# Performance work log

Measured on AMD Instinct MI355X. Metric: run time of the kernel, lower is better.

Reference implementation:

```python
import jax, jax.numpy as jnp
import numpy as np

B, C, H, W = 8, 128, 64, 64

def conv2d(x, w, b, pad):
    # x: [B,C,H,W], w: [O,I,kh,kw] -> NCHW conv with symmetric padding
    y = jax.lax.conv_general_dilated(
        x, w, window_strides=(1, 1), padding=[(pad, pad), (pad, pad)],
        dimension_numbers=("NCHW", "OIHW", "NCHW"))
    return y + b[None, :, None, None]

def setup_inputs() -> dict:
    key = jax.random.key(0)
    ks = jax.random.split(key, 5)
    s3 = 1.0 / np.sqrt(C * 9)  # kaiming-uniform-ish scale for 3x3 conv
    s1 = 1.0 / np.sqrt(C)
    return {
        "x": jax.random.normal(ks[0], (B, C, H, W), jnp.float32),
        "Wq": jax.random.normal(ks[1], (C, C, 3, 3), jnp.float32) * s3,
        "bq": jnp.zeros((C,), jnp.float32),
        "Wk": jax.random.normal(ks[2], (C, C, 3, 3), jnp.float32) * s3,
        "bk": jnp.zeros((C,), jnp.float32),
        "Wv": jax.random.normal(ks[3], (C, C, 3, 3), jnp.float32) * s3,
        "bv": jnp.zeros((C,), jnp.float32),
        "Wo": jax.random.normal(ks[4], (C, C, 1, 1), jnp.float32) * s1,
        "bo": jnp.zeros((C,), jnp.float32),
    }

def reference(x, Wq, bq, Wk, bk, Wv, bv, Wo, bo):
    b, c, h, w = x.shape
    n = h * w
    scale = c ** (-0.5)
    # NOTE: original module defines self.norm but never applies it in forward.
    q = conv2d(x, Wq, bq, 1).reshape(b, c, n)
    k = conv2d(x, Wk, bk, 1).reshape(b, c, n)
    v = conv2d(x, Wv, bv, 1).reshape(b, c, n)
    attn = jax.nn.softmax(jnp.einsum("bci,bcj->bij", q, k) * scale, axis=2)  # [b,n,n]
    out = jnp.einsum("bij,bcj->bci", attn, v).reshape(b, c, h, w)
    out = conv2d(out, Wo, bo, 0)
    return x + out
```

## Files before the change

### kernel.cpp

```cpp
#include <hip/hip_runtime.h>

typedef __attribute__((ext_vector_type(8))) short bf16x8;
typedef __attribute__((ext_vector_type(4))) float f32x4;
typedef __attribute__((ext_vector_type(16))) float f32x16;

static __device__ __forceinline__ unsigned short f2bf(float f) {
    union { float f; unsigned int u; } v; v.f = f;
    unsigned int r = v.u + 0x7FFFu + ((v.u >> 16) & 1u);
    return (unsigned short)(r >> 16);
}

static __device__ __forceinline__ unsigned cvtpk_bf16(float lo, float hi) {
    unsigned r;
    asm("v_cvt_pk_bf16_f32 %0, %1, %2" : "=v"(r) : "v"(lo), "v"(hi));
    return r;
}

#define NRW (27 * 16384)

__global__ __launch_bounds__(256) void repack_k(const float* __restrict__ Wq, const float* __restrict__ Wk,
                                                const float* __restrict__ Wv, const float* __restrict__ Wo,
                                                unsigned short* __restrict__ RW, unsigned short* __restrict__ WoB) {
    int t = blockIdx.x * 256 + threadIdx.x;
    if (t < NRW) {
        int s = t & 7, o = (t >> 3) & 127, g = (t >> 10) & 3, cc = (t >> 12) & 3, tap = t >> 14;
        int conv = tap / 9, kk = tap % 9, kh = kk / 3, kw = kk % 3;
        int c = cc * 32 + g * 8 + s;
        const float* W = (conv == 0) ? Wq : ((conv == 1) ? Wk : Wv);
        RW[t] = f2bf(W[((o * 128 + c) * 3 + kh) * 3 + kw]);
    } else {
        int u = t - NRW;
        if (u < 16384) WoB[u] = f2bf(Wo[u]);
    }
}

__global__ __launch_bounds__(256) void qkv_conv_k(const float* __restrict__ x, const unsigned short* __restrict__ RW,
                                                  const float* __restrict__ bq, const float* __restrict__ bk,
                                                  const float* __restrict__ bv,
                                                  unsigned short* __restrict__ q_ws, unsigned short* __restrict__ k_ws,
                                                  unsigned short* __restrict__ v_ws) {
    __shared__ unsigned short xs[3 * 66 * 128];
    const int tid = threadIdx.x;
    const int b = blockIdx.x >> 6, h = blockIdx.x & 63;
    for (int i = tid; i < 3 * 66 * 128; i += 256) xs[i] = 0;
    __syncthreads();
    for (int ch = tid; ch < 3 * 128 * 16; ch += 256) {
        int r3 = ch >> 11, rem = ch & 2047, c = rem >> 4, w4 = rem & 15;
        int hh = h - 1 + r3;
        if (hh >= 0 && hh < 64) {
            float4 v = *(const float4*)(x + ((b * 128 + c) * 64 + hh) * 64 + w4 * 4);
            float vv[4] = {v.x, v.y, v.z, v.w};
#pragma unroll
            for (int j = 0; j < 4; ++j) {
                int wr = w4 * 4 + j + 1;
                unsigned int byte = (unsigned int)(((r3 * 66 + wr) * 128 + c) * 2) ^ ((wr & 7) << 4);
                *(unsigned short*)((char*)xs + byte) = f2bf(vv[j]);
            }
        }
    }
    __syncthreads();
    const int lane = tid & 63, wave = tid >> 6;
    const int l15 = lane & 15, g = lane >> 4;
    f32x4 acc[4][6];
#pragma unroll
    for (int i = 0; i < 4; ++i)
#pragma unroll
        for (int j = 0; j < 6; ++j) acc[i][j] = (f32x4){0.f, 0.f, 0.f, 0.f};
#pragma unroll 1
    for (int kk = 0; kk < 9; ++kk) {
        const int kw = kk % 3;
#pragma unroll 2
        for (int cc = 0; cc < 4; ++cc) {
            bf16x8 a[4];
#pragma unroll
            for (int mf = 0; mf < 4; ++mf) {
                int wr = mf * 16 + l15 + kw;
                unsigned int byte = (unsigned int)((((kk / 3) * 66 + wr) * 128 + cc * 32 + g * 8) * 2) ^ ((wr & 7) << 4);
                a[mf] = *(const bf16x8*)((const char*)xs + byte);
            }
#pragma unroll
            for (int n6 = 0; n6 < 6; ++n6) {
                int nt = wave * 6 + n6;
                int conv = nt >> 3;
                int o = (nt * 16 + l15) & 127;
                bf16x8 bfr = *(const bf16x8*)(RW + ((((conv * 9 + kk) * 4 + cc) * 4 + g) * 128 + o) * 8);
#pragma unroll
                for (int mf = 0; mf < 4; ++mf)
                    acc[mf][n6] = __builtin_amdgcn_mfma_f32_16x16x32_bf16(a[mf], bfr, acc[mf][n6], 0, 0, 0);
            }
        }
    }
    const float SCALE2 = 0.08838834764831845f * 1.4426950408889634f;
#pragma unroll
    for (int n6 = 0; n6 < 6; ++n6) {
        int nt = wave * 6 + n6;
        int conv = nt >> 3;
        int o = (nt * 16 + l15) & 127;
        float bias = (conv == 0) ? bq[o] : ((conv == 1) ? bk[o] : bv[o]);
#pragma unroll
        for (int mf = 0; mf < 4; ++mf) {
#pragma unroll
            for (int r = 0; r < 4; ++r) {
                int pos = h * 64 + mf * 16 + g * 4 + r;
                float val = acc[mf][n6][r] + bias;
                if (conv == 0)      q_ws[(b * 4096 + pos) * 128 + o] = f2bf(val * SCALE2);
                else if (conv == 1) k_ws[(b * 4096 + pos) * 128 + o] = f2bf(val);
                else                v_ws[(b * 128 + o) * 4096 + pos] = f2bf(val);
            }
        }
    }
}

#define AS1C(p) ((const __attribute__((address_space(1))) void*)(p))
#define AS3(p)  ((__attribute__((address_space(3))) void*)(p))

__global__ __launch_bounds__(256, 2) void attn_k(
    const unsigned short* __restrict__ q_ws, const unsigned short* __restrict__ k_ws,
    const unsigned short* __restrict__ v_ws, const unsigned short* __restrict__ WoB,
    const float* __restrict__ bo, const float* __restrict__ x, float* __restrict__ out) {
    __shared__ __align__(16) char smem[66560];

    const int tid = threadIdx.x;
    const int lane = tid & 63, wave = tid >> 6;
    const int wj = wave & 1, wi = wave >> 1;
    const int l31 = lane & 31, h = lane >> 5;
    const int b = blockIdx.x & 7;
    const int qt = blockIdx.x >> 3;
    const int ibase = qt * 64;

    const char* kB = (const char*)(k_ws + (size_t)b * 4096 * 128);
    const char* vB = (const char*)(v_ws + (size_t)b * 128 * 4096);

    auto stage = [&](int buf, int kt) {
        char* Kn = smem + buf * 32768;
        char* Vn = Kn + 16384;
#pragma unroll
        for (int q = 0; q < 4; ++q) {
            int slot = (wave * 4 + q) * 64 + lane;
            int krow = slot >> 4, ks = slot & 15;
            int kcs = ks ^ (krow & 15);
            __builtin_amdgcn_global_load_lds(AS1C(kB + (size_t)(kt * 64 + krow) * 256 + kcs * 16),
                                             AS3(Kn + slot * 16), 16, 0, 0);
            int sr = slot >> 4, s8p = slot & 15;
            int s8 = s8p ^ (sr & 15);
            int crow = sr * 2 + (s8 >> 3), jch = s8 & 7;
            __builtin_amdgcn_global_load_lds(AS1C(vB + (size_t)crow * 8192 + kt * 128 + jch * 16),
                                             AS3(Vn + slot * 16), 16, 0, 0);
        }
    };

    stage(0, 0);

    bf16x8 qf[8];
    {
        const unsigned short* qrow = q_ws + ((size_t)b * 4096 + ibase + wi * 32 + l31) * 128;
#pragma unroll
        for (int cc = 0; cc < 8; ++cc) qf[cc] = *(const bf16x8*)(qrow + cc * 16 + h * 8);
    }

    f32x16 zero16;
#pragma unroll
    for (int r = 0; r < 16; ++r) zero16[r] = 0.f;
    f32x16 oac[4];
#pragma unroll
    for (int cf = 0; cf < 4; ++cf)
#pragma unroll
        for (int r = 0; r < 16; ++r) oac[cf][r] = 0.f;
    float m = -1e30f, ssum = 0.f;

    __syncthreads();

#pragma unroll 1
    for (int kt = 0; kt < 64; ++kt) {
        const int cur = kt & 1;
        const char* Kc = smem + cur * 32768;
        const char* Vc = Kc + 16384;
        if (kt < 63) stage(cur ^ 1, kt + 1);

        const int jrow = wj * 32 + l31;
        f32x16 st;
        __builtin_amdgcn_s_setprio(1);
        {
            unsigned byte = (unsigned)(jrow * 256 + ((h ^ (jrow & 15)) << 4));
            bf16x8 kf = *(const bf16x8*)(Kc + byte);
            st = __builtin_amdgcn_mfma_f32_32x32x16_bf16(kf, qf[0], zero16, 0, 0, 0);
        }
#pragma unroll
        for (int cc = 1; cc < 8; ++cc) {
            unsigned byte = (unsigned)(jrow * 256 + (((cc * 2 + h) ^ (jrow & 15)) << 4));
            bf16x8 kf = *(const bf16x8*)(Kc + byte);
            st = __builtin_amdgcn_mfma_f32_32x32x16_bf16(kf, qf[cc], st, 0, 0, 0);
        }
        __builtin_amdgcn_s_setprio(0);

        float x0 = fmaxf(fmaxf(st[0], st[1]), st[2]);
        float x1 = fmaxf(fmaxf(st[3], st[4]), st[5]);
        float x2 = fmaxf(fmaxf(st[6], st[7]), st[8]);
        float x3 = fmaxf(fmaxf(st[9], st[10]), st[11]);
        float x4 = fmaxf(fmaxf(st[12], st[13]), st[14]);
        float y0 = fmaxf(fmaxf(x0, x1), x2);
        float y1 = fmaxf(fmaxf(x3, x4), st[15]);
        float tmax = fmaxf(y0, y1);
        tmax = fmaxf(tmax, __shfl_xor(tmax, 32));
        if (!__all(tmax <= m + 8.f)) {
            float mnew = fmaxf(m, tmax);
            float corr = exp2f(m - mnew);
            ssum *= corr;
#pragma unroll
            for (int cf = 0; cf < 4; ++cf)
#pragma unroll
                for (int r = 0; r < 16; ++r) oac[cf][r] *= corr;
            m = mnew;
        }

        float ps = 0.f;
#pragma unroll
        for (int js = 0; js < 2; ++js) {
            float pA0 = exp2f(st[8 * js + 0] - m);
            float pA1 = exp2f(st[8 * js + 1] - m);
            float pA2 = exp2f(st[8 * js + 2] - m);
            float pA3 = exp2f(st[8 * js + 3] - m);
            float pB0 = exp2f(st[8 * js + 4] - m);
            float pB1 = exp2f(st[8 * js + 5] - m);
            float pB2 = exp2f(st[8 * js + 6] - m);
            float pB3 = exp2f(st[8 * js + 7] - m);
            ps += ((pA0 + pA1) + (pA2 + pA3)) + ((pB0 + pB1) + (pB2 + pB3));
            unsigned a0 = cvtpk_bf16(pA0, pA1), a1 = cvtpk_bf16(pA2, pA3);
            unsigned b0 = cvtpk_bf16(pB0, pB1), b1 = cvtpk_bf16(pB2, pB3);
            auto r0 = __builtin_amdgcn_permlane32_swap(a0, b0, false, false);
            auto r1 = __builtin_amdgcn_permlane32_swap(a1, b1, false, false);
            union { unsigned w[4]; bf16x8 v; } pu;
            pu.w[0] = r0[0];
            pu.w[1] = r1[0];
            pu.w[2] = r0[1];
            pu.w[3] = r1[1];
            const int jch = wj * 4 + js * 2 + h;
            __builtin_amdgcn_s_setprio(1);
#pragma unroll
            for (int cf = 0; cf < 4; ++cf) {
                int crow = cf * 32 + l31;
                int sr = crow >> 1;
                int s8 = ((crow & 1) << 3) | jch;
                unsigned vbyte = (unsigned)(sr * 256 + ((s8 ^ (sr & 15)) << 4));
                bf16x8 va = *(const bf16x8*)(Vc + vbyte);
                oac[cf] = __builtin_amdgcn_mfma_f32_32x32x16_bf16(va, pu.v, oac[cf], 0, 0, 0);
            }
            __builtin_amdgcn_s_setprio(0);
        }
        ps += __shfl_xor(ps, 32);
        ssum += ps;
        __syncthreads();
    }

    float* sRed = (float*)(smem + 65536);
    const int it = wi * 32 + l31;
    if (h == 0) {
        sRed[(wj * 64 + it) * 2] = m;
        sRed[(wj * 64 + it) * 2 + 1] = ssum;
    }
    __syncthreads();
    float m1 = sRed[((wj ^ 1) * 64 + it) * 2];
    float s1 = sRed[((wj ^ 1) * 64 + it) * 2 + 1];
    float M = fmaxf(m, m1);
    float aS = exp2f(m - M);
    float inv = 1.0f / (aS * ssum + exp2f(m1 - M) * s1);

    char* sBig = smem + 32768;
    if (wj == 1) {
#pragma unroll
        for (int cf = 0; cf < 4; ++cf)
#pragma unroll
            for (int g = 0; g < 4; ++g) {
                int c = cf * 32 + g * 8 + 4 * h;
                f32x4 v4;
#pragma unroll
                for (int k = 0; k < 4; ++k) v4[k] = aS * oac[cf][4 * g + k];
                unsigned byte = (unsigned)(it * 512 + c * 4) ^ ((it & 7) << 4);
                *(f32x4*)(sBig + byte) = v4;
            }
    }
    __syncthreads();
    unsigned short* sOut = (unsigned short*)smem;
    if (wj == 0) {
#pragma unroll
        for (int cf = 0; cf < 4; ++cf)
#pragma unroll
            for (int g = 0; g < 4; ++g) {
                int c = cf * 32 + g * 8 + 4 * h;
                unsigned rbyte = (unsigned)(it * 512 + c * 4) ^ ((it & 7) << 4);
                f32x4 rd = *(const f32x4*)((const char*)sBig + rbyte);
                float u0 = (aS * oac[cf][4 * g + 0] + rd[0]) * inv;
                float u1 = (aS * oac[cf][4 * g + 1] + rd[1]) * inv;
                float u2 = (aS * oac[cf][4 * g + 2] + rd[2]) * inv;
                float u3 = (aS * oac[cf][4 * g + 3] + rd[3]) * inv;
                uint2 pk;
                pk.x = cvtpk_bf16(u0, u1);
                pk.y = cvtpk_bf16(u2, u3);
                unsigned wbyte = (unsigned)(it * 256 + c * 2) ^ ((it & 15) << 4);
                *(uint2*)((char*)sOut + wbyte) = pk;
            }
    }
    __syncthreads();

#pragma unroll
    for (int t = 0; t < 2; ++t) {
        int tt = wave * 2 + t;
        int of = tt >> 1, ifl = tt & 1;
        int ir = ifl * 32 + l31;
        f32x16 acc;
#pragma unroll
        for (int r = 0; r < 16; ++r) acc[r] = 0.f;
#pragma unroll
        for (int cc = 0; cc < 8; ++cc) {
            unsigned bbyte = (unsigned)(ir * 256 + cc * 32 + h * 16) ^ ((ir & 15) << 4);
            bf16x8 bfr = *(const bf16x8*)((const char*)sOut + bbyte);
            bf16x8 wa = *(const bf16x8*)(WoB + (of * 32 + l31) * 128 + cc * 16 + h * 8);
            acc = __builtin_amdgcn_mfma_f32_32x32x16_bf16(wa, bfr, acc, 0, 0, 0);
        }
        int iglob = ibase + ir;
#pragma unroll
        for (int r = 0; r < 16; ++r) {
            int o = of * 32 + (r & 3) + 8 * (r >> 2) + 4 * h;
            size_t gidx = ((size_t)b * 128 + o) * 4096 + iglob;
            out[gidx] = acc[r] + bo[o] + x[gidx];
        }
    }
}

extern "C" void kernel_launch(void* const* d_in, const int* in_sizes, int n_in,
                              void* d_out, int out_size, void* d_ws, size_t ws_size,
                              hipStream_t stream) {
    const float* x  = (const float*)d_in[0];
    const float* Wq = (const float*)d_in[1];
    const float* bq = (const float*)d_in[2];
    const float* Wk = (const float*)d_in[3];
    const float* bk = (const float*)d_in[4];
    const float* Wv = (const float*)d_in[5];
    const float* bv = (const float*)d_in[6];
    const float* Wo = (const float*)d_in[7];
    const float* bo = (const float*)d_in[8];
    char* ws = (char*)d_ws;
    unsigned short* q_ws = (unsigned short*)(ws);
    unsigned short* k_ws = (unsigned short*)(ws + 8388608);
    unsigned short* v_ws = (unsigned short*)(ws + 16777216);
    unsigned short* RW   = (unsigned short*)(ws + 25165824);
    unsigned short* WoB  = (unsigned short*)(ws + 26050560);
    float* out = (float*)d_out;

    hipLaunchKernelGGL(repack_k, dim3(1792), dim3(256), 0, stream, Wq, Wk, Wv, Wo, RW, WoB);
    hipLaunchKernelGGL(qkv_conv_k, dim3(512), dim3(256), 0, stream, x, RW, bq, bk, bv, q_ws, k_ws, v_ws);
    hipLaunchKernelGGL(attn_k, dim3(512), dim3(256), 0, stream, q_ws, k_ws, v_ws, WoB, bo, x, out);
}
```

Measured before the change: 165.3 us.

## Software-pipeline QK^T one tile ahead and split K/V staging buffers

Restructures the attention loop so the QK^T MFMAs for tile kt+1 are issued before the softmax and PV work of tile kt. This gives the matrix units independent work to overlap with the exp and max VALU work. K is now prefetched two tiles ahead and V one tile ahead in separate double buffers, and the global addresses are precomputed once outside the loop. The s_setprio hints are removed. The change holds an extra 16-register score accumulator live, which raises register pressure and may limit occupancy at two blocks per CU.

```diff
diff --git a/kernel.cpp b/kernel.cpp
--- a/kernel.cpp
+++ b/kernel.cpp
@@ -131,25 +131,33 @@
     const char* kB = (const char*)(k_ws + (size_t)b * 4096 * 128);
     const char* vB = (const char*)(v_ws + (size_t)b * 128 * 4096);
 
-    auto stage = [&](int buf, int kt) {
-        char* Kn = smem + buf * 32768;
-        char* Vn = Kn + 16384;
-#pragma unroll
-        for (int q = 0; q < 4; ++q) {
-            int slot = (wave * 4 + q) * 64 + lane;
-            int krow = slot >> 4, ks = slot & 15;
-            int kcs = ks ^ (krow & 15);
-            __builtin_amdgcn_global_load_lds(AS1C(kB + (size_t)(kt * 64 + krow) * 256 + kcs * 16),
-                                             AS3(Kn + slot * 16), 16, 0, 0);
-            int sr = slot >> 4, s8p = slot & 15;
-            int s8 = s8p ^ (sr & 15);
-            int crow = sr * 2 + (s8 >> 3), jch = s8 & 7;
-            __builtin_amdgcn_global_load_lds(AS1C(vB + (size_t)crow * 8192 + kt * 128 + jch * 16),
-                                             AS3(Vn + slot * 16), 16, 0, 0);
-        }
+    const char* kgp[4]; const char* vgp[4]; int dst[4];
+#pragma unroll
+    for (int q = 0; q < 4; ++q) {
+        int slot = (wave * 4 + q) * 64 + lane;
+        int krow = slot >> 4, ks = slot & 15;
+        int kcs = ks ^ (krow & 15);
+        kgp[q] = kB + (size_t)krow * 256 + kcs * 16;
+        int sr = slot >> 4, s8p = slot & 15;
+        int s8 = s8p ^ (sr & 15);
+        int crow = sr * 2 + (s8 >> 3), jch = s8 & 7;
+        vgp[q] = vB + (size_t)crow * 8192 + jch * 16;
+        dst[q] = slot * 16;
+    }
+    auto stageK = [&](int buf, int kt) {
+#pragma unroll
+        for (int q = 0; q < 4; ++q)
+            __builtin_amdgcn_global_load_lds(AS1C(kgp[q] + (size_t)kt * 16384),
+                                             AS3(smem + buf * 16384 + dst[q]), 16, 0, 0);
     };
-
-    stage(0, 0);
+    auto stageV = [&](int buf, int kt) {
+#pragma unroll
+        for (int q = 0; q < 4; ++q)
+            __builtin_amdgcn_global_load_lds(AS1C(vgp[q] + (size_t)kt * 128),
+                                             AS3(smem + 32768 + buf * 16384 + dst[q]), 16, 0, 0);
+    };
+
+    stageK(0, 0); stageV(0, 0); stageK(1, 1);
 
     bf16x8 qf[8];
     {
@@ -168,38 +176,41 @@
         for (int r = 0; r < 16; ++r) oac[cf][r] = 0.f;
     float m = -1e30f, ssum = 0.f;
 
-    __syncthreads();
-
-#pragma unroll 1
-    for (int kt = 0; kt < 64; ++kt) {
-        const int cur = kt & 1;
-        const char* Kc = smem + cur * 32768;
-        const char* Vc = Kc + 16384;
-        if (kt < 63) stage(cur ^ 1, kt + 1);
-
-        const int jrow = wj * 32 + l31;
-        f32x16 st;
-        __builtin_amdgcn_s_setprio(1);
+    const int jrow = wj * 32 + l31;
+    auto QK = [&](const char* Kc) -> f32x16 {
+        f32x16 s;
         {
             unsigned byte = (unsigned)(jrow * 256 + ((h ^ (jrow & 15)) << 4));
             bf16x8 kf = *(const bf16x8*)(Kc + byte);
-            st = __builtin_amdgcn_mfma_f32_32x32x16_bf16(kf, qf[0], zero16, 0, 0, 0);
+            s = __builtin_amdgcn_mfma_f32_32x32x16_bf16(kf, qf[0], zero16, 0, 0, 0);
         }
 #pragma unroll
         for (int cc = 1; cc < 8; ++cc) {
             unsigned byte = (unsigned)(jrow * 256 + (((cc * 2 + h) ^ (jrow & 15)) << 4));
             bf16x8 kf = *(const bf16x8*)(Kc + byte);
-            st = __builtin_amdgcn_mfma_f32_32x32x16_bf16(kf, qf[cc], st, 0, 0, 0);
-        }
-        __builtin_amdgcn_s_setprio(0);
-
-        float x0 = fmaxf(fmaxf(st[0], st[1]), st[2]);
-        float x1 = fmaxf(fmaxf(st[3], st[4]), st[5]);
-        float x2 = fmaxf(fmaxf(st[6], st[7]), st[8]);
-        float x3 = fmaxf(fmaxf(st[9], st[10]), st[11]);
-        float x4 = fmaxf(fmaxf(st[12], st[13]), st[14]);
+            s = __builtin_amdgcn_mfma_f32_32x32x16_bf16(kf, qf[cc], s, 0, 0, 0);
+        }
+        return s;
+    };
+
+    __syncthreads();
+
+    f32x16 stp = QK(smem);
+
+#pragma unroll 1
+    for (int kt = 0; kt < 64; ++kt) {
+        if (kt < 62) stageK(kt & 1, kt + 2);
+        if (kt < 63) stageV((kt + 1) & 1, kt + 1);
+        f32x16 stn;
+        if (kt < 63) stn = QK(smem + ((kt + 1) & 1) * 16384);
+
+        float x0 = fmaxf(fmaxf(stp[0], stp[1]), stp[2]);
+        float x1 = fmaxf(fmaxf(stp[3], stp[4]), stp[5]);
+        float x2 = fmaxf(fmaxf(stp[6], stp[7]), stp[8]);
+        float x3 = fmaxf(fmaxf(stp[9], stp[10]), stp[11]);
+        float x4 = fmaxf(fmaxf(stp[12], stp[13]), stp[14]);
         float y0 = fmaxf(fmaxf(x0, x1), x2);
-        float y1 = fmaxf(fmaxf(x3, x4), st[15]);
+        float y1 = fmaxf(fmaxf(x3, x4), stp[15]);
         float tmax = fmaxf(y0, y1);
         tmax = fmaxf(tmax, __shfl_xor(tmax, 32));
         if (!__all(tmax <= m + 8.f)) {
@@ -213,17 +224,18 @@
             m = mnew;
         }
 
+        const char* Vc = smem + 32768 + (kt & 1) * 16384;
         float ps = 0.f;
 #pragma unroll
         for (int js = 0; js < 2; ++js) {
-            float pA0 = exp2f(st[8 * js + 0] - m);
-            float pA1 = exp2f(st[8 * js + 1] - m);
-            float pA2 = exp2f(st[8 * js + 2] - m);
-            float pA3 = exp2f(st[8 * js + 3] - m);
-            float pB0 = exp2f(st[8 * js + 4] - m);
-            float pB1 = exp2f(st[8 * js + 5] - m);
-            float pB2 = exp2f(st[8 * js + 6] - m);
-            float pB3 = exp2f(st[8 * js + 7] - m);
+            float pA0 = exp2f(stp[8 * js + 0] - m);
+            float pA1 = exp2f(stp[8 * js + 1] - m);
+            float pA2 = exp2f(stp[8 * js + 2] - m);
+            float pA3 = exp2f(stp[8 * js + 3] - m);
+            float pB0 = exp2f(stp[8 * js + 4] - m);
+            float pB1 = exp2f(stp[8 * js + 5] - m);
+            float pB2 = exp2f(stp[8 * js + 6] - m);
+            float pB3 = exp2f(stp[8 * js + 7] - m);
             ps += ((pA0 + pA1) + (pA2 + pA3)) + ((pB0 + pB1) + (pB2 + pB3));
             unsigned a0 = cvtpk_bf16(pA0, pA1), a1 = cvtpk_bf16(pA2, pA3);
             unsigned b0 = cvtpk_bf16(pB0, pB1), b1 = cvtpk_bf16(pB2, pB3);
@@ -235,7 +247,6 @@
             pu.w[2] = r0[1];
             pu.w[3] = r1[1];
             const int jch = wj * 4 + js * 2 + h;
-            __builtin_amdgcn_s_setprio(1);
 #pragma unroll
             for (int cf = 0; cf < 4; ++cf) {
                 int crow = cf * 32 + l31;
@@ -245,10 +256,10 @@
                 bf16x8 va = *(const bf16x8*)(Vc + vbyte);
                 oac[cf] = __builtin_amdgcn_mfma_f32_32x32x16_bf16(va, pu.v, oac[cf], 0, 0, 0);
             }
-            __builtin_amdgcn_s_setprio(0);
         }
         ps += __shfl_xor(ps, 32);
         ssum += ps;
+        stp = stn;
         __syncthreads();
     }
 
```

New measurement: 165.5 us. About the same (+0.1%).

## Load K and V fragments directly from global memory instead of LDS staging

Applied to the files above, without the earlier changes.

Removes the double-buffered global_load_lds staging of K and V tiles into shared memory, along with the per-iteration barrier and the s_setprio hints. Each lane now reads its K and V MFMA fragments straight from global memory. Shared memory shrinks to cover only the epilogue reduction and output buffers. This drops the barriers and LDS traffic, but the loads are no longer prefetched, so global and L2 latency sits in the critical path, and the V reads are strided small-chunk accesses.

```diff
diff --git a/kernel.cpp b/kernel.cpp
--- a/kernel.cpp
+++ b/kernel.cpp
@@ -111,14 +111,11 @@
     }
 }
 
-#define AS1C(p) ((const __attribute__((address_space(1))) void*)(p))
-#define AS3(p)  ((__attribute__((address_space(3))) void*)(p))
-
 __global__ __launch_bounds__(256, 2) void attn_k(
     const unsigned short* __restrict__ q_ws, const unsigned short* __restrict__ k_ws,
     const unsigned short* __restrict__ v_ws, const unsigned short* __restrict__ WoB,
     const float* __restrict__ bo, const float* __restrict__ x, float* __restrict__ out) {
-    __shared__ __align__(16) char smem[66560];
+    __shared__ __align__(16) char smem[50176];
 
     const int tid = threadIdx.x;
     const int lane = tid & 63, wave = tid >> 6;
@@ -131,25 +128,12 @@
     const char* kB = (const char*)(k_ws + (size_t)b * 4096 * 128);
     const char* vB = (const char*)(v_ws + (size_t)b * 128 * 4096);
 
-    auto stage = [&](int buf, int kt) {
-        char* Kn = smem + buf * 32768;
-        char* Vn = Kn + 16384;
-#pragma unroll
-        for (int q = 0; q < 4; ++q) {
-            int slot = (wave * 4 + q) * 64 + lane;
-            int krow = slot >> 4, ks = slot & 15;
-            int kcs = ks ^ (krow & 15);
-            __builtin_amdgcn_global_load_lds(AS1C(kB + (size_t)(kt * 64 + krow) * 256 + kcs * 16),
-                                             AS3(Kn + slot * 16), 16, 0, 0);
-            int sr = slot >> 4, s8p = slot & 15;
-            int s8 = s8p ^ (sr & 15);
-            int crow = sr * 2 + (s8 >> 3), jch = s8 & 7;
-            __builtin_amdgcn_global_load_lds(AS1C(vB + (size_t)crow * 8192 + kt * 128 + jch * 16),
-                                             AS3(Vn + slot * 16), 16, 0, 0);
-        }
-    };
-
-    stage(0, 0);
+    const int jrow = wj * 32 + l31;
+    const char* kRow = kB + (size_t)jrow * 256 + h * 16;
+    const char* vRow[4];
+#pragma unroll
+    for (int cf = 0; cf < 4; ++cf)
+        vRow[cf] = vB + (size_t)(cf * 32 + l31) * 8192 + (wj * 4 + h) * 16;
 
     bf16x8 qf[8];
     {
@@ -168,30 +152,20 @@
         for (int r = 0; r < 16; ++r) oac[cf][r] = 0.f;
     float m = -1e30f, ssum = 0.f;
 
-    __syncthreads();
-
 #pragma unroll 1
     for (int kt = 0; kt < 64; ++kt) {
-        const int cur = kt & 1;
-        const char* Kc = smem + cur * 32768;
-        const char* Vc = Kc + 16384;
-        if (kt < 63) stage(cur ^ 1, kt + 1);
-
-        const int jrow = wj * 32 + l31;
+        const char* Kc = kRow + (size_t)kt * 16384;
+
         f32x16 st;
-        __builtin_amdgcn_s_setprio(1);
         {
-            unsigned byte = (unsigned)(jrow * 256 + ((h ^ (jrow & 15)) << 4));
-            bf16x8 kf = *(const bf16x8*)(Kc + byte);
+            bf16x8 kf = *(const bf16x8*)(Kc);
             st = __builtin_amdgcn_mfma_f32_32x32x16_bf16(kf, qf[0], zero16, 0, 0, 0);
         }
 #pragma unroll
         for (int cc = 1; cc < 8; ++cc) {
-            unsigned byte = (unsigned)(jrow * 256 + (((cc * 2 + h) ^ (jrow & 15)) << 4));
-            bf16x8 kf = *(const bf16x8*)(Kc + byte);
+            bf16x8 kf = *(const bf16x8*)(Kc + cc * 32);
             st = __builtin_amdgcn_mfma_f32_32x32x16_bf16(kf, qf[cc], st, 0, 0, 0);
         }
-        __builtin_amdgcn_s_setprio(0);
 
         float x0 = fmaxf(fmaxf(st[0], st[1]), st[2]);
         float x1 = fmaxf(fmaxf(st[3], st[4]), st[5]);
@@ -234,25 +208,17 @@
             pu.w[1] = r1[0];
             pu.w[2] = r0[1];
             pu.w[3] = r1[1];
-            const int jch = wj * 4 + js * 2 + h;
-            __builtin_amdgcn_s_setprio(1);
 #pragma unroll
             for (int cf = 0; cf < 4; ++cf) {
-                int crow = cf * 32 + l31;
-                int sr = crow >> 1;
-                int s8 = ((crow & 1) << 3) | jch;
-                unsigned vbyte = (unsigned)(sr * 256 + ((s8 ^ (sr & 15)) << 4));
-                bf16x8 va = *(const bf16x8*)(Vc + vbyte);
+                bf16x8 va = *(const bf16x8*)(vRow[cf] + (size_t)kt * 128 + js * 32);
                 oac[cf] = __builtin_amdgcn_mfma_f32_32x32x16_bf16(va, pu.v, oac[cf], 0, 0, 0);
             }
-            __builtin_amdgcn_s_setprio(0);
         }
         ps += __shfl_xor(ps, 32);
         ssum += ps;
-        __syncthreads();
-    }
-
-    float* sRed = (float*)(smem + 65536);
+    }
+
+    float* sRed = (float*)(smem + 49152);
     const int it = wi * 32 + l31;
     if (h == 0) {
         sRed[(wj * 64 + it) * 2] = m;
@@ -265,7 +231,7 @@
     float aS = exp2f(m - M);
     float inv = 1.0f / (aS * ssum + exp2f(m1 - M) * s1);
 
-    char* sBig = smem + 32768;
+    char* sBig = smem;
     if (wj == 1) {
 #pragma unroll
         for (int cf = 0; cf < 4; ++cf)
@@ -280,7 +246,7 @@
             }
     }
     __syncthreads();
-    unsigned short* sOut = (unsigned short*)smem;
+    unsigned short* sOut = (unsigned short*)(smem + 32768);
     if (wj == 0) {
 #pragma unroll
         for (int cf = 0; cf < 4; ++cf)
```

Measured after the change: 295.7 us. 1.79x slower.

## Split attention PV output channels across two extra waves per block

Applied to the files above, without the earlier changes.

Doubles the attention block from 4 to 8 waves, adding a channel-split index so each wave accumulates only half of the 128 output channels in the P·V step. The QK^T score and softmax work is now duplicated across the channel-split wave pairs, while per-wave accumulator registers are halved and staging work per wave drops. The LDS layout is reorganised so K and V buffers are separated, and the final normalisation is folded into a single combined scale. The intent is more waves in flight to hide latency, at the cost of redundant score MFMAs and the same LDS per block.

```diff
diff --git a/kernel.cpp b/kernel.cpp
--- a/kernel.cpp
+++ b/kernel.cpp
@@ -114,29 +114,28 @@
 #define AS1C(p) ((const __attribute__((address_space(1))) void*)(p))
 #define AS3(p)  ((__attribute__((address_space(3))) void*)(p))
 
-__global__ __launch_bounds__(256, 2) void attn_k(
+__global__ __launch_bounds__(512, 4) void attn_k(
     const unsigned short* __restrict__ q_ws, const unsigned short* __restrict__ k_ws,
     const unsigned short* __restrict__ v_ws, const unsigned short* __restrict__ WoB,
     const float* __restrict__ bo, const float* __restrict__ x, float* __restrict__ out) {
-    __shared__ __align__(16) char smem[66560];
+    __shared__ __align__(16) char smem[67584];
 
     const int tid = threadIdx.x;
     const int lane = tid & 63, wave = tid >> 6;
-    const int wj = wave & 1, wi = wave >> 1;
+    const int wc = wave & 1, wj = (wave >> 1) & 1, wi = wave >> 2;
     const int l31 = lane & 31, h = lane >> 5;
     const int b = blockIdx.x & 7;
-    const int qt = blockIdx.x >> 3;
-    const int ibase = qt * 64;
+    const int ibase = (blockIdx.x >> 3) * 64;
 
     const char* kB = (const char*)(k_ws + (size_t)b * 4096 * 128);
     const char* vB = (const char*)(v_ws + (size_t)b * 128 * 4096);
 
     auto stage = [&](int buf, int kt) {
-        char* Kn = smem + buf * 32768;
-        char* Vn = Kn + 16384;
-#pragma unroll
-        for (int q = 0; q < 4; ++q) {
-            int slot = (wave * 4 + q) * 64 + lane;
+        char* Kn = smem + buf * 16384;
+        char* Vn = smem + 32768 + buf * 16384;
+#pragma unroll
+        for (int q = 0; q < 2; ++q) {
+            int slot = (wave * 2 + q) * 64 + lane;
             int krow = slot >> 4, ks = slot & 15;
             int kcs = ks ^ (krow & 15);
             __builtin_amdgcn_global_load_lds(AS1C(kB + (size_t)(kt * 64 + krow) * 256 + kcs * 16),
@@ -161,23 +160,24 @@
     f32x16 zero16;
 #pragma unroll
     for (int r = 0; r < 16; ++r) zero16[r] = 0.f;
-    f32x16 oac[4];
-#pragma unroll
-    for (int cf = 0; cf < 4; ++cf)
+    f32x16 oac[2];
+#pragma unroll
+    for (int cf = 0; cf < 2; ++cf)
 #pragma unroll
         for (int r = 0; r < 16; ++r) oac[cf][r] = 0.f;
     float m = -1e30f, ssum = 0.f;
+
+    const int jrow = wj * 32 + l31;
 
     __syncthreads();
 
 #pragma unroll 1
     for (int kt = 0; kt < 64; ++kt) {
         const int cur = kt & 1;
-        const char* Kc = smem + cur * 32768;
-        const char* Vc = Kc + 16384;
+        const char* Kc = smem + cur * 16384;
+        const char* Vc = smem + 32768 + cur * 16384;
         if (kt < 63) stage(cur ^ 1, kt + 1);
 
-        const int jrow = wj * 32 + l31;
         f32x16 st;
         __builtin_amdgcn_s_setprio(1);
         {
@@ -207,7 +207,7 @@
             float corr = exp2f(m - mnew);
             ssum *= corr;
 #pragma unroll
-            for (int cf = 0; cf < 4; ++cf)
+            for (int cf = 0; cf < 2; ++cf)
 #pragma unroll
                 for (int r = 0; r < 16; ++r) oac[cf][r] *= corr;
             m = mnew;
@@ -237,8 +237,8 @@
             const int jch = wj * 4 + js * 2 + h;
             __builtin_amdgcn_s_setprio(1);
 #pragma unroll
-            for (int cf = 0; cf < 4; ++cf) {
-                int crow = cf * 32 + l31;
+            for (int cf = 0; cf < 2; ++cf) {
+                int crow = (wc * 2 + cf) * 32 + l31;
                 int sr = crow >> 1;
                 int s8 = ((crow & 1) << 3) | jch;
                 unsigned vbyte = (unsigned)(sr * 256 + ((s8 ^ (sr & 15)) << 4));
@@ -254,58 +254,61 @@
 
     float* sRed = (float*)(smem + 65536);
     const int it = wi * 32 + l31;
-    if (h == 0) {
+    if (wc == 0 && h == 0) {
         sRed[(wj * 64 + it) * 2] = m;
         sRed[(wj * 64 + it) * 2 + 1] = ssum;
     }
     __syncthreads();
-    float m1 = sRed[((wj ^ 1) * 64 + it) * 2];
-    float s1 = sRed[((wj ^ 1) * 64 + it) * 2 + 1];
-    float M = fmaxf(m, m1);
-    float aS = exp2f(m - M);
-    float inv = 1.0f / (aS * ssum + exp2f(m1 - M) * s1);
-
-    char* sBig = smem + 32768;
+    float aS;
+    {
+        float m0 = sRed[(0 * 64 + it) * 2], s0 = sRed[(0 * 64 + it) * 2 + 1];
+        float m1 = sRed[(1 * 64 + it) * 2], s1 = sRed[(1 * 64 + it) * 2 + 1];
+        float M = fmaxf(m0, m1);
+        float stot = exp2f(m0 - M) * s0 + exp2f(m1 - M) * s1;
+        aS = exp2f(m - M) / stot;
+    }
+    __syncthreads();
+
+    char* sBig = smem + wc * 16384;
     if (wj == 1) {
 #pragma unroll
-        for (int cf = 0; cf < 4; ++cf)
+        for (int cf = 0; cf < 2; ++cf)
 #pragma unroll
             for (int g = 0; g < 4; ++g) {
-                int c = cf * 32 + g * 8 + 4 * h;
+                int c2 = cf * 32 + g * 8 + 4 * h;
                 f32x4 v4;
 #pragma unroll
                 for (int k = 0; k < 4; ++k) v4[k] = aS * oac[cf][4 * g + k];
-                unsigned byte = (unsigned)(it * 512 + c * 4) ^ ((it & 7) << 4);
+                unsigned byte = (unsigned)(it * 256 + c2 * 4) ^ ((it & 15) << 4);
                 *(f32x4*)(sBig + byte) = v4;
             }
     }
     __syncthreads();
-    unsigned short* sOut = (unsigned short*)smem;
+    unsigned short* sOut = (unsigned short*)(smem + 32768);
     if (wj == 0) {
 #pragma unroll
-        for (int cf = 0; cf < 4; ++cf)
+        for (int cf = 0; cf < 2; ++cf)
 #pragma unroll
             for (int g = 0; g < 4; ++g) {
-                int c = cf * 32 + g * 8 + 4 * h;
-                unsigned rbyte = (unsigned)(it * 512 + c * 4) ^ ((it & 7) << 4);
+                int c2 = cf * 32 + g * 8 + 4 * h;
+                unsigned rbyte = (unsigned)(it * 256 + c2 * 4) ^ ((it & 15) << 4);
                 f32x4 rd = *(const f32x4*)((const char*)sBig + rbyte);
-                float u0 = (aS * oac[cf][4 * g + 0] + rd[0]) * inv;
-                float u1 = (aS * oac[cf][4 * g + 1] + rd[1]) * inv;
-                float u2 = (aS * oac[cf][4 * g + 2] + rd[2]) * inv;
-                float u3 = (aS * oac[cf][4 * g + 3] + rd[3]) * inv;
+                float u0 = aS * oac[cf][4 * g + 0] + rd[0];
+                float u1 = aS * oac[cf][4 * g + 1] + rd[1];
+                float u2 = aS * oac[cf][4 * g + 2] + rd[2];
+                float u3 = aS * oac[cf][4 * g + 3] + rd[3];
                 uint2 pk;
                 pk.x = cvtpk_bf16(u0, u1);
                 pk.y = cvtpk_bf16(u2, u3);
+                int c = wc * 64 + c2;
                 unsigned wbyte = (unsigned)(it * 256 + c * 2) ^ ((it & 15) << 4);
                 *(uint2*)((char*)sOut + wbyte) = pk;
             }
     }
     __syncthreads();
 
-#pragma unroll
-    for (int t = 0; t < 2; ++t) {
-        int tt = wave * 2 + t;
-        int of = tt >> 1, ifl = tt & 1;
+    {
+        int of = wave >> 1, ifl = wave & 1;
         int ir = ifl * 32 + l31;
         f32x16 acc;
 #pragma unroll
@@ -349,5 +352,5 @@
 
     hipLaunchKernelGGL(repack_k, dim3(1792), dim3(256), 0, stream, Wq, Wk, Wv, Wo, RW, WoB);
     hipLaunchKernelGGL(qkv_conv_k, dim3(512), dim3(256), 0, stream, x, RW, bq, bk, bv, q_ws, k_ws, v_ws);
-    hipLaunchKernelGGL(attn_k, dim3(512), dim3(256), 0, stream, q_ws, k_ws, v_ws, WoB, bo, x, out);
-}
+    hipLaunchKernelGGL(attn_k, dim3(512), dim3(512), 0, stream, q_ws, k_ws, v_ws, WoB, bo, x, out);
+}
```

New measurement: 207.0 us. 1.25x slower.
